# Performance work log

Hardware: AMD Instinct MI355X
Metric: run time of the kernel (lower is better)

The kernel has to match this reference:

```python
import jax, jax.numpy as jnp
from jax import lax
import numpy as np

N_SPLITS = 2
N_LEVELS = 3
B, T, C = 32, 1024, 128
HID = 512          # int(input_dim * hidden_size) = 128 * 4
K1, K2 = 5, 3      # first conv kernel_size, second conv kernel=3
N_INTER = 7        # 1 + 2 + 4 interactors in the binary tree
LEAKY_SLOPE = 0.01


def setup_inputs() -> dict:
    key = jax.random.key(0)
    ks = jax.random.split(key, 9)
    w = 0.05  # small init so exp-gating stays well-conditioned
    return {
        "x": jax.random.normal(ks[0], (B, T, C), jnp.float32),
        "mul_w1": jax.random.normal(ks[1], (N_INTER, N_SPLITS, K1, C, HID), jnp.float32) * w,
        "mul_b1": jnp.zeros((N_INTER, N_SPLITS, HID), jnp.float32),
        "mul_w2": jax.random.normal(ks[2], (N_INTER, N_SPLITS, K2, HID, C), jnp.float32) * w,
        "mul_b2": jnp.zeros((N_INTER, N_SPLITS, C), jnp.float32),
        "add_w1": jax.random.normal(ks[3], (N_INTER, N_SPLITS, K1, C, HID), jnp.float32) * w,
        "add_b1": jnp.zeros((N_INTER, N_SPLITS, HID), jnp.float32),
        "add_w2": jax.random.normal(ks[4], (N_INTER, N_SPLITS, K2, HID, C), jnp.float32) * w,
        "add_b2": jnp.zeros((N_INTER, N_SPLITS, C), jnp.float32),
    }


def _leaky(x):
    return jnp.where(x > 0, x, LEAKY_SLOPE * x)


def _causal_conv(x, w, b):
    # x: [B, L, Cin], w: [K, Cin, Cout] (keras WIO layout); 'causal' = left-pad K-1
    k = w.shape[0]
    y = lax.conv_general_dilated(x, w, window_strides=(1,),
                                 padding=[(k - 1, 0)],
                                 dimension_numbers=("NWC", "WIO", "NWC"))
    return y + b


def _conv_seq(x, w1, b1, w2, b2):
    # Conv1D(causal, LeakyReLU 0.01) -> Dropout(identity at inference) -> Conv1D(k=3, causal, tanh)
    h = _leaky(_causal_conv(x, w1, b1))
    return jnp.tanh(_causal_conv(h, w2, b2))


def _interactor(x, idx, p):
    # x: [B, L, C]; strided temporal split into N_SPLITS pieces of length L//N_SPLITS
    splits = [x[:, i::N_SPLITS, :] for i in range(N_SPLITS)]
    scale = N_SPLITS - 1
    mul_list = []
    for i in range(N_SPLITS):
        s = 0.0
        for j in range(N_SPLITS):
            if j != i:
                s = s + _conv_seq(splits[j], p["mul_w1"][idx, i], p["mul_b1"][idx, i],
                                  p["mul_w2"][idx, i], p["mul_b2"][idx, i])
        # prod_j exp(f(x_j)) ** (1/scale) == exp(sum_j f(x_j) / scale)
        mul_list.append(splits[i] * jnp.exp(s / scale))
    out = []
    for i in range(N_SPLITS):
        a = 0.0
        for j in range(N_SPLITS):
            if j != i:
                a = a + _conv_seq(mul_list[j], p["add_w1"][idx, i], p["add_b1"][idx, i],
                                  p["add_w2"][idx, i], p["add_b2"][idx, i])
        a = a / scale
        out.append(mul_list[i] + a if i % 2 == 0 else mul_list[i] - a)
    return out


def reference(x, mul_w1, mul_b1, mul_w2, mul_b2, add_w1, add_b1, add_w2, add_b2):
    p = {"mul_w1": mul_w1, "mul_b1": mul_b1, "mul_w2": mul_w2, "mul_b2": mul_b2,
         "add_w1": add_w1, "add_b1": add_b1, "add_w2": add_w2, "add_b2": add_b2}
    t_in = x.shape[1]
    min_unit = N_SPLITS ** N_LEVELS
    pad = (-t_in) % min_unit  # left zero-pad to a multiple of n_splits**n_levels
    xp = jnp.pad(x, ((0, 0), (pad, 0), (0, 0)))
    seq = [xp]
    idx = 0
    for lvl in range(N_LEVELS):
        nxt = []
        for j in range(N_SPLITS ** lvl):
            nxt += _interactor(seq[j], idx, p)
            idx += 1
        seq = nxt
    # rev_split: recursively concatenate along time with stride `steps`
    while len(seq) > 1:
        steps = len(seq) // N_SPLITS
        seq = [jnp.concatenate([seq[i + s * steps] for s in range(N_SPLITS)], axis=1)
               for i in range(steps)]
    return seq[0][:, -t_in:, :]
```

## Files before the change

### kernel.cpp

```cpp
#include <hip/hip_runtime.h>
#include <hip/hip_bf16.h>
#include <stdint.h>


static constexpr int B_ = 32, T_ = 1024, C_ = 128, HID_ = 512;
static constexpr int K1_ = 5, K2_ = 3;

typedef __attribute__((ext_vector_type(8))) _Float16 half8;
typedef __attribute__((ext_vector_type(4))) float f32x4;

__device__ __forceinline__ unsigned short f2h(float f) {
    _Float16 h = (_Float16)f;
    return __builtin_bit_cast(unsigned short, h);
}

__device__ __forceinline__ void gload16(const void* g, void* l) {
    __builtin_amdgcn_global_load_lds(
        (const __attribute__((address_space(1))) unsigned int*)g,
        (__attribute__((address_space(3))) unsigned int*)l, 16, 0, 0);
}

template<int CIN, int COUT>
__global__ __launch_bounds__(256)
void wprep_k(const float* __restrict__ win1, unsigned short* __restrict__ wout1,
             const float* __restrict__ win2, unsigned short* __restrict__ wout2,
             int nhalf) {
    constexpr int TA = CIN / 64, TB = COUT / 64;
    int blk = blockIdx.x;
    int tb = blk % TB;
    int ta = (blk / TB) % TA;
    int s  = blk / (TA * TB);
    const float* win;
    unsigned short* wout;
    if (s < nhalf) { win = win1; wout = wout1; }
    else           { win = win2; wout = wout2; s -= nhalf; }
    __shared__ float tile[64][65];
    const float* src = win + (size_t)s * CIN * COUT;
    unsigned short* dst = wout + (size_t)s * CIN * COUT;
    int cl = threadIdx.x & 63;
    int rw = threadIdx.x >> 6;
    for (int r = rw; r < 64; r += 4)
        tile[r][cl] = src[(size_t)(ta * 64 + r) * COUT + tb * 64 + cl];
    __syncthreads();
    for (int r = rw; r < 64; r += 4) {
        int co = tb * 64 + r;
        int ci = ta * 64 + cl;
        int ciw = (ci & ~127) | ((ci & 127) ^ ((co & 7) << 3));
        dst[(size_t)co * CIN + ciw] = f2h(tile[cl][r]);
    }
}

__global__ __launch_bounds__(256)
void split_k(const float* __restrict__ cur, unsigned short* __restrict__ outb,
             int Ls) {
    int idx = blockIdx.x * 256 + threadIdx.x;
    int row = idx >> 5;
    int cq  = (idx & 31) << 2;
    int BLs = B_ * Ls;
    int g  = row / BLs;
    int r2 = row - g * BLs;
    int b  = r2 / Ls;
    int u  = r2 - b * Ls;
    int p = g >> 1, i = g & 1;
    const float4 v = *(const float4*)(cur +
        ((size_t)(p * B_ + b) * (2 * Ls) + 2 * u + i) * C_ + cq);
    ushort4 o;
    o.x = f2h(v.x); o.y = f2h(v.y); o.z = f2h(v.z); o.w = f2h(v.w);
    int cqw = cq ^ (((u + 4) & 7) << 3);
    *(ushort4*)(outb + (size_t)row * C_ + cqw) = o;
}

__global__ __launch_bounds__(256, 2)
void conv1_k(const unsigned short* __restrict__ actb,
             const unsigned short* __restrict__ wT,
             const float* __restrict__ bias,
             unsigned short* __restrict__ hid,
             const unsigned short* __restrict__ zp,
             int Ls, int RT, int idxbase) {
    __shared__ unsigned short smemA[132 * 128];
    __shared__ unsigned short smemB[2][64 * 128];

    const int tid = threadIdx.x;
    const int lane = tid & 63;
    const int w = tid >> 6;
    const int wr = w >> 1, wc = w & 1;

    int blk = blockIdx.x;
    const int ct = blk & 7;
    int t1 = blk >> 3;
    const int rt = t1 % RT;
    const int g  = t1 / RT;
    const int n0 = ct * 64;
    const int rowstart = rt * 128;
    const int b  = rowstart / Ls;
    const int t0 = rowstart - b * Ls;

    const int gin  = g ^ 1;
    const int widx = (idxbase + (g >> 1)) * 2 + (g & 1);

    const char* inb = (const char*)(actb + (size_t)(gin * B_ + b) * Ls * C_);
    const char* wb  = (const char*)(wT + (size_t)widx * (K1_ * HID_ * C_));
    const float* bptr = bias + (size_t)widx * HID_;

    const int bq  = lane * 16;
    const int bco = bq >> 8;
    const int bcb = bq & 255;

#pragma unroll
    for (int ch0 = 0; ch0 < 4; ++ch0) {
        int ch = w + ch0 * 4;
        gload16(wb + (size_t)(n0 + ch * 4 + bco) * 256 + bcb,
                (char*)smemB[0] + ch * 1024);
    }
    for (int ch = w; ch < 33; ch += 4) {
        int q = ch * 1024 + lane * 16;
        int r = q >> 8;
        int cb = q & 255;
        int t = t0 - 4 + r;
        const char* src = (t >= 0) ? inb + (size_t)t * 256 + cb
                                   : (const char*)zp + cb;
        gload16(src, (char*)smemA + ch * 1024);
    }
    asm volatile("s_waitcnt vmcnt(0)" ::: "memory");
    __syncthreads();

    f32x4 acc[4][2];
#pragma unroll
    for (int m = 0; m < 4; ++m)
#pragma unroll
        for (int n = 0; n < 2; ++n) acc[m][n] = (f32x4){0.f, 0.f, 0.f, 0.f};

#pragma unroll
    for (int kk = 0; kk < K1_; ++kk) {
        if (kk < K1_ - 1) {
            const char* wt = wb + (size_t)(kk + 1) * HID_ * C_ * 2;
#pragma unroll
            for (int ch0 = 0; ch0 < 4; ++ch0) {
                int ch = w + ch0 * 4;
                gload16(wt + (size_t)(n0 + ch * 4 + bco) * 256 + bcb,
                        (char*)smemB[(kk + 1) & 1] + ch * 1024);
            }
        }
        const unsigned short* sB = smemB[kk & 1];
#pragma unroll
        for (int ks = 0; ks < 4; ++ks) {
            half8 aF[4], bF[2];
            const int cole = ks * 32 + ((lane >> 4) << 3);
#pragma unroll
            for (int m = 0; m < 4; ++m) {
                int ar = kk + wr * 64 + m * 16 + (lane & 15);
                aF[m] = *(const half8*)(smemA + ar * 128 + (cole ^ ((ar & 7) << 3)));
            }
#pragma unroll
            for (int n = 0; n < 2; ++n) {
                int br = wc * 32 + n * 16 + (lane & 15);
                bF[n] = *(const half8*)(sB + br * 128 + (cole ^ ((br & 7) << 3)));
            }
#pragma unroll
            for (int m = 0; m < 4; ++m) {
                acc[m][0] = __builtin_amdgcn_mfma_f32_16x16x32_f16(
                    aF[m], bF[0], acc[m][0], 0, 0, 0);
                acc[m][1] = __builtin_amdgcn_mfma_f32_16x16x32_f16(
                    aF[m], bF[1], acc[m][1], 0, 0, 0);
            }
        }
        if (kk < K1_ - 1) __syncthreads();
    }

    unsigned short* outp = hid + ((size_t)(g * B_ + b) * Ls + t0) * HID_;
#pragma unroll
    for (int n = 0; n < 2; ++n) {
        int co = n0 + wc * 32 + n * 16 + (lane & 15);
        float bv = bptr[co];
#pragma unroll
        for (int m = 0; m < 4; ++m) {
            int u0 = wr * 64 + m * 16 + ((lane >> 4) << 2);
#pragma unroll
            for (int q = 0; q < 4; ++q) {
                float v = acc[m][n][q] + bv;
                v = (v > 0.f) ? v : 0.01f * v;
                int t = t0 + u0 + q;
                int cow = (co & ~127) | ((co & 127) ^ (((t + 2) & 7) << 3));
                outp[(size_t)(u0 + q) * HID_ + cow] = f2h(v);
            }
        }
    }
}

template<int EPI>
__global__ __launch_bounds__(256, 3)
void conv2_k(const unsigned short* __restrict__ hid,
             const unsigned short* __restrict__ wT,
             const float* __restrict__ bias,
             const float* __restrict__ cur,
             float* __restrict__ mulf,
             unsigned short* __restrict__ actb,
             float* __restrict__ nxt,
             unsigned short* __restrict__ actn,
             float* __restrict__ dout,
             const unsigned short* __restrict__ zp,
             int Ls, int RT, int idxbase) {
    __shared__ unsigned short smemA[66 * 128];
    __shared__ unsigned short smemB[128 * 128];

    const int tid = threadIdx.x;
    const int lane = tid & 63;
    const int w = tid >> 6;
    const int wr = w >> 1, wc = w & 1;

    int blk = blockIdx.x;
    const int rt = blk % RT;
    const int g  = blk / RT;
    const int rowstart = rt * 64;
    const int b  = rowstart / Ls;
    const int t0 = rowstart - b * Ls;
    const int widx = (idxbase + (g >> 1)) * 2 + (g & 1);

    const char* inb = (const char*)(hid + (size_t)(g * B_ + b) * Ls * HID_);
    const char* wb  = (const char*)(wT + (size_t)widx * (K2_ * C_ * HID_));
    const float* bptr = bias + (size_t)widx * C_;

    f32x4 acc[2][4];
#pragma unroll
    for (int m = 0; m < 2; ++m)
#pragma unroll
        for (int n = 0; n < 4; ++n) acc[m][n] = (f32x4){0.f, 0.f, 0.f, 0.f};

    for (int ck = 0; ck < 4; ++ck) {
        if (ck) __syncthreads();
        for (int ch = w; ch < 17; ch += 4) {
            int q = ch * 1024 + lane * 16;
            if (q < 16896) {
                int r = q >> 8;
                int cb = q & 255;
                int t = t0 - 2 + r;
                const char* src = (t >= 0)
                    ? inb + (size_t)t * 1024 + ck * 256 + cb
                    : (const char*)zp + cb;
                gload16(src, (char*)smemA + ch * 1024);
            }
        }
        for (int kk = 0; kk < K2_; ++kk) {
            if (kk) __syncthreads();
            const char* wt = wb + (size_t)kk * C_ * HID_ * 2;
            for (int ch = w; ch < 32; ch += 4) {
                int q = ch * 1024 + lane * 16;
                int co = q >> 8;
                int cb = q & 255;
                gload16(wt + (size_t)co * 1024 + ck * 256 + cb,
                        (char*)smemB + ch * 1024);
            }
            asm volatile("s_waitcnt vmcnt(0)" ::: "memory");
            __syncthreads();

#pragma unroll
            for (int ks = 0; ks < 4; ++ks) {
                half8 aF[2], bF[4];
                const int cole = ks * 32 + ((lane >> 4) << 3);
#pragma unroll
                for (int m = 0; m < 2; ++m) {
                    int ar = kk + wr * 32 + m * 16 + (lane & 15);
                    aF[m] = *(const half8*)(smemA + ar * 128 + (cole ^ ((ar & 7) << 3)));
                }
#pragma unroll
                for (int n = 0; n < 4; ++n) {
                    int br = wc * 64 + n * 16 + (lane & 15);
                    bF[n] = *(const half8*)(smemB + br * 128 + (cole ^ ((br & 7) << 3)));
                }
#pragma unroll
                for (int m = 0; m < 2; ++m)
#pragma unroll
                    for (int n = 0; n < 4; ++n)
                        acc[m][n] = __builtin_amdgcn_mfma_f32_16x16x32_f16(
                            aF[m], bF[n], acc[m][n], 0, 0, 0);
            }
        }
    }

    const size_t rowb = (size_t)(g * B_ + b) * Ls + t0;
    const int p_ = g >> 1, i_ = g & 1;
    const int Ls2 = Ls >> 1;
#pragma unroll
    for (int n = 0; n < 4; ++n) {
        int c = wc * 64 + n * 16 + (lane & 15);
        float bv = bptr[c];
#pragma unroll
        for (int m = 0; m < 2; ++m) {
            int u0 = wr * 32 + m * 16 + ((lane >> 4) << 2);
#pragma unroll
            for (int q = 0; q < 4; ++q) {
                float v = acc[m][n][q] + bv;
                float xc = fminf(fmaxf(v, -15.f), 15.f);
                float e2 = __expf(2.f * xc);
                float th = (e2 - 1.f) / (e2 + 1.f);
                size_t ro = rowb + (size_t)(u0 + q);
                int u = t0 + u0 + q;
                if (EPI == 0) {
                    float sv = cur[((size_t)(p_ * B_ + b) * (2 * Ls) + 2 * u + i_) * C_ + c];
                    float mv = sv * __expf(th);
                    mulf[ro * C_ + c] = mv;
                    int cw = c ^ (((u + 4) & 7) << 3);
                    actb[ro * C_ + cw] = f2h(mv);
                } else {
                    float mv = mulf[ro * C_ + c];
                    float val = (i_ == 0) ? (mv + th) : (mv - th);
                    if (EPI == 1) {
                        nxt[ro * C_ + c] = val;
                        int gq = g * 2 + (u & 1);
                        int uq = u >> 1;
                        int cw = c ^ (((uq + 4) & 7) << 3);
                        actn[((size_t)(gq * B_ + b) * Ls2 + uq) * C_ + cw] = f2h(val);
                    } else {
                        int tau = u | (((g >> 2) & 1) << 7) | (((g >> 1) & 1) << 8)
                                    | ((g & 1) << 9);
                        dout[((size_t)b * T_ + tau) * C_ + c] = val;
                    }
                }
            }
        }
    }
}

extern "C" void kernel_launch(void* const* d_in, const int* in_sizes, int n_in,
                              void* d_out, int out_size, void* d_ws, size_t ws_size,
                              hipStream_t stream) {
    const float* x   = (const float*)d_in[0];
    const float* mw1 = (const float*)d_in[1];
    const float* mb1 = (const float*)d_in[2];
    const float* mw2 = (const float*)d_in[3];
    const float* mb2 = (const float*)d_in[4];
    const float* aw1 = (const float*)d_in[5];
    const float* ab1 = (const float*)d_in[6];
    const float* aw2 = (const float*)d_in[7];
    const float* ab2 = (const float*)d_in[8];

    char* ws = (char*)d_ws;
    size_t off = 0;
    auto alloc = [&](size_t sz) {
        char* p = ws + off;
        off += (sz + 255) & ~(size_t)255;
        return p;
    };
    unsigned short* zp   = (unsigned short*)alloc(8192);
    unsigned short* w1m  = (unsigned short*)alloc((size_t)14 * 5 * 512 * 128 * 2);
    unsigned short* w1a  = (unsigned short*)alloc((size_t)14 * 5 * 512 * 128 * 2);
    unsigned short* w2m  = (unsigned short*)alloc((size_t)14 * 3 * 128 * 512 * 2);
    unsigned short* w2a  = (unsigned short*)alloc((size_t)14 * 3 * 128 * 512 * 2);
    float* bufA          = (float*)alloc((size_t)4194304 * 4);
    float* bufB          = (float*)alloc((size_t)4194304 * 4);
    unsigned short* actb = (unsigned short*)alloc((size_t)4194304 * 2);
    unsigned short* hidb = (unsigned short*)alloc((size_t)16777216 * 2);
    float* mulf          = (float*)alloc((size_t)4194304 * 4);
    (void)ws_size; (void)n_in; (void)in_sizes; (void)out_size;

    hipMemsetAsync(zp, 0, 8192, stream);

    wprep_k<128, 512><<<2240, 256, 0, stream>>>(mw1, w1m, aw1, w1a, 70);
    wprep_k<512, 128><<<1344, 256, 0, stream>>>(mw2, w2m, aw2, w2a, 42);

    split_k<<<4096, 256, 0, stream>>>(x, actb, 512);

    for (int lvl = 0; lvl < 3; ++lvl) {
        const int P = 1 << lvl;
        const int G = 2 * P;
        const int Ls = (1024 >> lvl) >> 1;
        const int idxbase = P - 1;
        const float* cur = (lvl == 0) ? x : ((lvl == 1) ? bufA : bufB);
        float* nxt = (lvl == 1) ? bufB : bufA;
        const int RT1 = Ls / 4;
        const int RT2 = Ls / 2;

        conv1_k<<<G * RT1 * 8, 256, 0, stream>>>(actb, w1m, mb1, hidb, zp,
                                                 Ls, RT1, idxbase);
        conv2_k<0><<<G * RT2, 256, 0, stream>>>(hidb, w2m, mb2, cur, mulf,
                                                actb, nullptr, nullptr, nullptr,
                                                zp, Ls, RT2, idxbase);
        conv1_k<<<G * RT1 * 8, 256, 0, stream>>>(actb, w1a, ab1, hidb, zp,
                                                 Ls, RT1, idxbase);
        if (lvl < 2) {
            conv2_k<1><<<G * RT2, 256, 0, stream>>>(hidb, w2a, ab2, nullptr, mulf,
                                                    nullptr, nxt, actb, nullptr,
                                                    zp, Ls, RT2, idxbase);
        } else {
            conv2_k<2><<<G * RT2, 256, 0, stream>>>(hidb, w2a, ab2, nullptr, mulf,
                                                    nullptr, nullptr, nullptr,
                                                    (float*)d_out,
                                                    zp, Ls, RT2, idxbase);
        }
    }
}
```

Baseline: 378.6 us.

## Move weight double-buffering from conv1 to conv2 and split conv2 output channels

conv1 drops its double-buffered weight staging in favour of a single buffer with a synchronous load per tap, and its occupancy hint rises from 2 to 3 blocks. conv2 is split into two 64-channel halves per row tile, doubling its grid. It now double-buffers its weight tiles across the (chunk, tap) loop so the next tile is prefetched during the MFMAs. The aim is to hide conv2's load latency and add parallelism, at the cost of exposed weight-load stalls in conv1 and conv2 re-reading its activation tile once per channel half.

```diff
diff --git a/kernel.cpp b/kernel.cpp
--- a/kernel.cpp
+++ b/kernel.cpp
@@ -70,7 +70,7 @@
     *(ushort4*)(outb + (size_t)row * C_ + cqw) = o;
 }
 
-__global__ __launch_bounds__(256, 2)
+__global__ __launch_bounds__(256, 3)
 void conv1_k(const unsigned short* __restrict__ actb,
              const unsigned short* __restrict__ wT,
              const float* __restrict__ bias,
@@ -78,7 +78,7 @@
              const unsigned short* __restrict__ zp,
              int Ls, int RT, int idxbase) {
     __shared__ unsigned short smemA[132 * 128];
-    __shared__ unsigned short smemB[2][64 * 128];
+    __shared__ unsigned short smemB[64 * 128];
 
     const int tid = threadIdx.x;
     const int lane = tid & 63;
@@ -102,16 +102,6 @@
     const char* wb  = (const char*)(wT + (size_t)widx * (K1_ * HID_ * C_));
     const float* bptr = bias + (size_t)widx * HID_;
 
-    const int bq  = lane * 16;
-    const int bco = bq >> 8;
-    const int bcb = bq & 255;
-
-#pragma unroll
-    for (int ch0 = 0; ch0 < 4; ++ch0) {
-        int ch = w + ch0 * 4;
-        gload16(wb + (size_t)(n0 + ch * 4 + bco) * 256 + bcb,
-                (char*)smemB[0] + ch * 1024);
-    }
     for (int ch = w; ch < 33; ch += 4) {
         int q = ch * 1024 + lane * 16;
         int r = q >> 8;
@@ -121,8 +111,6 @@
                                    : (const char*)zp + cb;
         gload16(src, (char*)smemA + ch * 1024);
     }
-    asm volatile("s_waitcnt vmcnt(0)" ::: "memory");
-    __syncthreads();
 
     f32x4 acc[4][2];
 #pragma unroll
@@ -130,18 +118,18 @@
 #pragma unroll
         for (int n = 0; n < 2; ++n) acc[m][n] = (f32x4){0.f, 0.f, 0.f, 0.f};
 
-#pragma unroll
     for (int kk = 0; kk < K1_; ++kk) {
-        if (kk < K1_ - 1) {
-            const char* wt = wb + (size_t)(kk + 1) * HID_ * C_ * 2;
-#pragma unroll
-            for (int ch0 = 0; ch0 < 4; ++ch0) {
-                int ch = w + ch0 * 4;
-                gload16(wt + (size_t)(n0 + ch * 4 + bco) * 256 + bcb,
-                        (char*)smemB[(kk + 1) & 1] + ch * 1024);
-            }
-        }
-        const unsigned short* sB = smemB[kk & 1];
+        if (kk) __syncthreads();
+        const char* wt = wb + (size_t)kk * HID_ * C_ * 2;
+        for (int ch = w; ch < 16; ch += 4) {
+            int q = ch * 1024 + lane * 16;
+            int co = q >> 8;
+            int cb = q & 255;
+            gload16(wt + (size_t)(n0 + co) * 256 + cb, (char*)smemB + ch * 1024);
+        }
+        asm volatile("s_waitcnt vmcnt(0)" ::: "memory");
+        __syncthreads();
+
 #pragma unroll
         for (int ks = 0; ks < 4; ++ks) {
             half8 aF[4], bF[2];
@@ -154,7 +142,7 @@
 #pragma unroll
             for (int n = 0; n < 2; ++n) {
                 int br = wc * 32 + n * 16 + (lane & 15);
-                bF[n] = *(const half8*)(sB + br * 128 + (cole ^ ((br & 7) << 3)));
+                bF[n] = *(const half8*)(smemB + br * 128 + (cole ^ ((br & 7) << 3)));
             }
 #pragma unroll
             for (int m = 0; m < 4; ++m) {
@@ -164,7 +152,6 @@
                     aF[m], bF[1], acc[m][1], 0, 0, 0);
             }
         }
-        if (kk < K1_ - 1) __syncthreads();
     }
 
     unsigned short* outp = hid + ((size_t)(g * B_ + b) * Ls + t0) * HID_;
@@ -201,7 +188,7 @@
              const unsigned short* __restrict__ zp,
              int Ls, int RT, int idxbase) {
     __shared__ unsigned short smemA[66 * 128];
-    __shared__ unsigned short smemB[128 * 128];
+    __shared__ unsigned short smemB[2][64 * 128];
 
     const int tid = threadIdx.x;
     const int lane = tid & 63;
@@ -209,8 +196,11 @@
     const int wr = w >> 1, wc = w & 1;
 
     int blk = blockIdx.x;
-    const int rt = blk % RT;
-    const int g  = blk / RT;
+    const int ct = blk & 1;
+    int t1 = blk >> 1;
+    const int rt = t1 % RT;
+    const int g  = t1 / RT;
+    const int n0 = ct * 64;
     const int rowstart = rt * 64;
     const int b  = rowstart / Ls;
     const int t0 = rowstart - b * Ls;
@@ -220,14 +210,11 @@
     const char* wb  = (const char*)(wT + (size_t)widx * (K2_ * C_ * HID_));
     const float* bptr = bias + (size_t)widx * C_;
 
-    f32x4 acc[2][4];
-#pragma unroll
-    for (int m = 0; m < 2; ++m)
-#pragma unroll
-        for (int n = 0; n < 4; ++n) acc[m][n] = (f32x4){0.f, 0.f, 0.f, 0.f};
-
-    for (int ck = 0; ck < 4; ++ck) {
-        if (ck) __syncthreads();
+    const int bq  = lane * 16;
+    const int bco = bq >> 8;
+    const int bcb = bq & 255;
+
+    auto stageA = [&](int ck) {
         for (int ch = w; ch < 17; ch += 4) {
             int q = ch * 1024 + lane * 16;
             if (q < 16896) {
@@ -240,22 +227,41 @@
                 gload16(src, (char*)smemA + ch * 1024);
             }
         }
+    };
+    auto stageB = [&](int ck, int kk, int buf) {
+        const char* wt = wb + (size_t)kk * C_ * HID_ * 2;
+#pragma unroll
+        for (int ch0 = 0; ch0 < 4; ++ch0) {
+            int ch = w + ch0 * 4;
+            gload16(wt + (size_t)(n0 + ch * 4 + bco) * 1024 + ck * 256 + bcb,
+                    (char*)smemB[buf] + ch * 1024);
+        }
+    };
+
+    f32x4 acc[2][2];
+#pragma unroll
+    for (int m = 0; m < 2; ++m)
+#pragma unroll
+        for (int n = 0; n < 2; ++n) acc[m][n] = (f32x4){0.f, 0.f, 0.f, 0.f};
+
+    stageB(0, 0, 0);
+    stageA(0);
+    asm volatile("s_waitcnt vmcnt(0)" ::: "memory");
+    __syncthreads();
+
+#pragma unroll
+    for (int ck = 0; ck < 4; ++ck) {
+#pragma unroll
         for (int kk = 0; kk < K2_; ++kk) {
-            if (kk) __syncthreads();
-            const char* wt = wb + (size_t)kk * C_ * HID_ * 2;
-            for (int ch = w; ch < 32; ch += 4) {
-                int q = ch * 1024 + lane * 16;
-                int co = q >> 8;
-                int cb = q & 255;
-                gload16(wt + (size_t)co * 1024 + ck * 256 + cb,
-                        (char*)smemB + ch * 1024);
-            }
-            asm volatile("s_waitcnt vmcnt(0)" ::: "memory");
-            __syncthreads();
-
+            const int r = ck * 3 + kk;
+            if (r < 11) {
+                if (kk < 2) stageB(ck, kk + 1, (r + 1) & 1);
+                else        stageB(ck + 1, 0, (r + 1) & 1);
+            }
+            const unsigned short* sB = smemB[r & 1];
 #pragma unroll
             for (int ks = 0; ks < 4; ++ks) {
-                half8 aF[2], bF[4];
+                half8 aF[2], bF[2];
                 const int cole = ks * 32 + ((lane >> 4) << 3);
 #pragma unroll
                 for (int m = 0; m < 2; ++m) {
@@ -263,16 +269,24 @@
                     aF[m] = *(const half8*)(smemA + ar * 128 + (cole ^ ((ar & 7) << 3)));
                 }
 #pragma unroll
-                for (int n = 0; n < 4; ++n) {
-                    int br = wc * 64 + n * 16 + (lane & 15);
-                    bF[n] = *(const half8*)(smemB + br * 128 + (cole ^ ((br & 7) << 3)));
+                for (int n = 0; n < 2; ++n) {
+                    int br = wc * 32 + n * 16 + (lane & 15);
+                    bF[n] = *(const half8*)(sB + br * 128 + (cole ^ ((br & 7) << 3)));
                 }
 #pragma unroll
                 for (int m = 0; m < 2; ++m)
 #pragma unroll
-                    for (int n = 0; n < 4; ++n)
+                    for (int n = 0; n < 2; ++n)
                         acc[m][n] = __builtin_amdgcn_mfma_f32_16x16x32_f16(
                             aF[m], bF[n], acc[m][n], 0, 0, 0);
+            }
+            if (r < 11) {
+                if (kk == 2) {
+                    __syncthreads();
+                    stageA(ck + 1);
+                }
+                asm volatile("s_waitcnt vmcnt(0)" ::: "memory");
+                __syncthreads();
             }
         }
     }
@@ -281,8 +295,8 @@
     const int p_ = g >> 1, i_ = g & 1;
     const int Ls2 = Ls >> 1;
 #pragma unroll
-    for (int n = 0; n < 4; ++n) {
-        int c = wc * 64 + n * 16 + (lane & 15);
+    for (int n = 0; n < 2; ++n) {
+        int c = n0 + wc * 32 + n * 16 + (lane & 15);
         float bv = bptr[c];
 #pragma unroll
         for (int m = 0; m < 2; ++m) {
@@ -372,20 +386,20 @@
 
         conv1_k<<<G * RT1 * 8, 256, 0, stream>>>(actb, w1m, mb1, hidb, zp,
                                                  Ls, RT1, idxbase);
-        conv2_k<0><<<G * RT2, 256, 0, stream>>>(hidb, w2m, mb2, cur, mulf,
-                                                actb, nullptr, nullptr, nullptr,
-                                                zp, Ls, RT2, idxbase);
+        conv2_k<0><<<G * RT2 * 2, 256, 0, stream>>>(hidb, w2m, mb2, cur, mulf,
+                                                    actb, nullptr, nullptr, nullptr,
+                                                    zp, Ls, RT2, idxbase);
         conv1_k<<<G * RT1 * 8, 256, 0, stream>>>(actb, w1a, ab1, hidb, zp,
                                                  Ls, RT1, idxbase);
         if (lvl < 2) {
-            conv2_k<1><<<G * RT2, 256, 0, stream>>>(hidb, w2a, ab2, nullptr, mulf,
-                                                    nullptr, nxt, actb, nullptr,
-                                                    zp, Ls, RT2, idxbase);
+            conv2_k<1><<<G * RT2 * 2, 256, 0, stream>>>(hidb, w2a, ab2, nullptr, mulf,
+                                                        nullptr, nxt, actb, nullptr,
+                                                        zp, Ls, RT2, idxbase);
         } else {
-            conv2_k<2><<<G * RT2, 256, 0, stream>>>(hidb, w2a, ab2, nullptr, mulf,
-                                                    nullptr, nullptr, nullptr,
-                                                    (float*)d_out,
-                                                    zp, Ls, RT2, idxbase);
-        }
-    }
-}
+            conv2_k<2><<<G * RT2 * 2, 256, 0, stream>>>(hidb, w2a, ab2, nullptr, mulf,
+                                                        nullptr, nullptr, nullptr,
+                                                        (float*)d_out,
+                                                        zp, Ls, RT2, idxbase);
+        }
+    }
+}
```

Result: slower. 411.5 us (+8.7%).
